# Kernel tuning notes

Measured on AMD Instinct MI355X. Metric: run time of the kernel, lower is better.

Reference implementation:

```python
import jax, jax.numpy as jnp
import numpy as np
import math

N, IN, OUT, E, K = 50000, 256, 256, 800000, 32

def setup_inputs() -> dict:
    key = jax.random.key(0)
    k0, k1, k2, k3, k4 = jax.random.split(key, 5)
    feat = jax.random.normal(k0, (N, IN), dtype=jnp.float32)
    # xavier_uniform with relu gain, as in reset_parameters
    gain = math.sqrt(2.0)
    a = gain * math.sqrt(6.0 / (IN + OUT))
    W_self = jax.random.uniform(k1, (OUT, IN), minval=-a, maxval=a, dtype=jnp.float32)
    W_neigh = jax.random.uniform(k2, (OUT, IN), minval=-a, maxval=a, dtype=jnp.float32)
    b_neigh = jnp.zeros((OUT,), dtype=jnp.float32)
    # random CSR graph: E edges, row pointers from sorted cut points
    indices = jax.random.randint(k3, (E,), 0, N, dtype=jnp.int32)
    inner = jnp.sort(jax.random.randint(k4, (N - 1,), 0, E, dtype=jnp.int32))
    indptr = jnp.concatenate([jnp.zeros((1,), jnp.int32), inner,
                              jnp.full((1,), E, jnp.int32)])
    return {"feat": feat, "W_self": W_self, "W_neigh": W_neigh,
            "b_neigh": b_neigh, "indices": indices, "indptr": indptr}

def reference(feat, W_self, W_neigh, b_neigh, indices, indptr):
    n = feat.shape[0]
    # feat_drop with p=0.0 is identity
    h_self = feat @ W_self.T                      # [N, OUT]
    feat_neigh = feat @ W_neigh.T + b_neigh       # [N, OUT]
    # MaxK: keep top-k entries per row, zero the rest
    vals, idx = jax.lax.top_k(feat_neigh, K)      # [N, K]
    rows = jnp.arange(n)[:, None]
    masked = jnp.zeros_like(feat_neigh).at[rows, idx].set(vals)
    # CSR SpMM with unit values (sum over neighbors)
    deg = indptr[1:] - indptr[:-1]                # [N]
    dst = jnp.repeat(jnp.arange(n, dtype=jnp.int32), deg,
                     total_repeat_length=indices.shape[0])
    h_neigh = jax.ops.segment_sum(masked[indices], dst, num_segments=n)
    return h_self + h_neigh
```

## Files before the change

### kernel.cpp

```cpp
#include <hip/hip_runtime.h>

#define N_NODES 50000
#define TOPK 32
#define SOFT_DELTA 2e-5f

typedef unsigned long long u64;
typedef unsigned u32;
typedef float f32x16 __attribute__((ext_vector_type(16)));
typedef __bf16 bf16x8 __attribute__((ext_vector_type(8)));

__device__ __forceinline__ float dec(u32 u) {
    return __builtin_bit_cast(float, (u & 0x80000000u) ? (u & 0x7FFFFFFFu) : ~u);
}
__device__ __forceinline__ int mbcnt64(u64 m) {
    return __builtin_amdgcn_mbcnt_hi((u32)(m >> 32),
           __builtin_amdgcn_mbcnt_lo((u32)m, 0u));
}

__device__ __forceinline__ u32 enc4(float v, int col) {
    return ((u32)col << 16) |
           ((__builtin_bit_cast(u32, v) + 0x8000u) >> 16);
}

__device__ __forceinline__ u32 s2(float x0, float x1, float& r0, float& r1) {
    const u32 h0 = (__builtin_bit_cast(u32, x0) + 0x8000u) & 0xFFFF0000u;
    const u32 h1 = (__builtin_bit_cast(u32, x1) + 0x8000u) & 0xFFFF0000u;
    r0 = x0 - __builtin_bit_cast(float, h0);
    r1 = x1 - __builtin_bit_cast(float, h1);
    return (h0 >> 16) | h1;
}
__device__ __forceinline__ u32 p2(float x0, float x1) {
    return (((__builtin_bit_cast(u32, x0) + 0x8000u) & 0xFFFF0000u) >> 16) |
           ((__builtin_bit_cast(u32, x1) + 0x8000u) & 0xFFFF0000u);
}

struct Tri { uint4 h1, h2, h3; };
__device__ __forceinline__ Tri cvt8(const float4 u, const float4 v, bool deep) {
    Tri t;
    float r0,r1,r2,r3,r4,r5,r6,r7;
    t.h1.x = s2(u.x, u.y, r0, r1);
    t.h1.y = s2(u.z, u.w, r2, r3);
    t.h1.z = s2(v.x, v.y, r4, r5);
    t.h1.w = s2(v.z, v.w, r6, r7);
    float s0,s1,s2_,s3,s4,s5,s6,s7;
    t.h2.x = s2(r0, r1, s0, s1);
    t.h2.y = s2(r2, r3, s2_, s3);
    t.h2.z = s2(r4, r5, s4, s5);
    t.h2.w = s2(r6, r7, s6, s7);
    if (deep) {
        t.h3.x = p2(s0, s1); t.h3.y = p2(s2_, s3);
        t.h3.z = p2(s4, s5); t.h3.w = p2(s6, s7);
    } else {
        t.h3 = make_uint4(0, 0, 0, 0);
    }
    return t;
}

__global__ __launch_bounds__(256, 2) void gemm_kernel(
    const float* __restrict__ feat,
    const float* __restrict__ Wself,
    const float* __restrict__ Wneigh,
    const float* __restrict__ bneigh,
    float* __restrict__ hself,
    float* __restrict__ fneigh)
{
    __shared__ uint4 LA1[512], LA2[512], LA3[512];
    __shared__ uint4 LB1[512], LB2[512], LB3[512];

    const int tid  = threadIdx.x;
    const int lane = tid & 63;
    const int wave = tid >> 6;
    const int wm   = wave >> 1;
    const int wn   = wave & 1;
    const int kg   = lane >> 5;

    const int rowTile = blockIdx.x >> 2;
    const int colTile = blockIdx.x & 3;
    const int row0 = rowTile * 128;
    const float* __restrict__ Wbase = (colTile < 2) ? Wself : Wneigh;
    const int jbase = (colTile & 1) << 7;
    const bool deep = (colTile >= 2);

    const int srow  = tid >> 1;
    const int shalf = tid & 1;
    int gra = row0 + srow;
    if (gra >= N_NODES) gra = 0;
    const float* pa = feat  + (size_t)gra * 256 + shalf * 16;
    const float* pb = Wbase + (size_t)(jbase + srow) * 256 + shalf * 16;
    const int i0 = ((shalf * 2) << 7) + srow;
    const int i1 = i0 + 128;

    const int rA0 = wm * 64 + (lane & 31);
    const int rB0 = wn * 64 + (lane & 31);

    f32x16 acc[2][2];
#pragma unroll
    for (int i = 0; i < 2; ++i)
#pragma unroll
        for (int j = 0; j < 2; ++j) acc[i][j] = (f32x16)0.f;

    float4 va0, va1, va2, va3, vb0, vb1, vb2, vb3;
    va0 = *(const float4*)(pa);      va1 = *(const float4*)(pa + 4);
    va2 = *(const float4*)(pa + 8);  va3 = *(const float4*)(pa + 12);
    vb0 = *(const float4*)(pb);      vb1 = *(const float4*)(pb + 4);
    vb2 = *(const float4*)(pb + 8);  vb3 = *(const float4*)(pb + 12);

    for (int s = 0; s < 8; ++s) {
        __syncthreads();
        {
            const Tri tA0 = cvt8(va0, va1, deep);
            const Tri tA1 = cvt8(va2, va3, deep);
            const Tri tB0 = cvt8(vb0, vb1, deep);
            const Tri tB1 = cvt8(vb2, vb3, deep);
            LA1[i0] = tA0.h1; LA2[i0] = tA0.h2;
            LA1[i1] = tA1.h1; LA2[i1] = tA1.h2;
            LB1[i0] = tB0.h1; LB2[i0] = tB0.h2;
            LB1[i1] = tB1.h1; LB2[i1] = tB1.h2;
            if (deep) {
                LA3[i0] = tA0.h3; LA3[i1] = tA1.h3;
                LB3[i0] = tB0.h3; LB3[i1] = tB1.h3;
            }
        }
        __syncthreads();

        if (s < 7) {
            const int ko = (s + 1) * 32;
            va0 = *(const float4*)(pa + ko);      va1 = *(const float4*)(pa + ko + 4);
            va2 = *(const float4*)(pa + ko + 8);  va3 = *(const float4*)(pa + ko + 12);
            vb0 = *(const float4*)(pb + ko);      vb1 = *(const float4*)(pb + ko + 4);
            vb2 = *(const float4*)(pb + ko + 8);  vb3 = *(const float4*)(pb + ko + 12);
        }

        if (deep) {
#pragma unroll
            for (int ks = 0; ks < 2; ++ks) {
                const int base = ((ks << 1) | kg) << 7;
                bf16x8 a1[2], a2[2], a3[2], b1[2], b2[2], b3[2];
#pragma unroll
                for (int f = 0; f < 2; ++f) {
                    const int ia = base + rA0 + f * 32;
                    const int ib = base + rB0 + f * 32;
                    a1[f] = __builtin_bit_cast(bf16x8, LA1[ia]);
                    a2[f] = __builtin_bit_cast(bf16x8, LA2[ia]);
                    a3[f] = __builtin_bit_cast(bf16x8, LA3[ia]);
                    b1[f] = __builtin_bit_cast(bf16x8, LB1[ib]);
                    b2[f] = __builtin_bit_cast(bf16x8, LB2[ib]);
                    b3[f] = __builtin_bit_cast(bf16x8, LB3[ib]);
                }
#pragma unroll
                for (int i = 0; i < 2; ++i)
#pragma unroll
                    for (int j = 0; j < 2; ++j) {
                        acc[i][j] = __builtin_amdgcn_mfma_f32_32x32x16_bf16(
                            a1[i], b1[j], acc[i][j], 0, 0, 0);
                        acc[i][j] = __builtin_amdgcn_mfma_f32_32x32x16_bf16(
                            a1[i], b2[j], acc[i][j], 0, 0, 0);
                        acc[i][j] = __builtin_amdgcn_mfma_f32_32x32x16_bf16(
                            a2[i], b1[j], acc[i][j], 0, 0, 0);
                        acc[i][j] = __builtin_amdgcn_mfma_f32_32x32x16_bf16(
                            a2[i], b2[j], acc[i][j], 0, 0, 0);
                        acc[i][j] = __builtin_amdgcn_mfma_f32_32x32x16_bf16(
                            a1[i], b3[j], acc[i][j], 0, 0, 0);
                        acc[i][j] = __builtin_amdgcn_mfma_f32_32x32x16_bf16(
                            a3[i], b1[j], acc[i][j], 0, 0, 0);
                    }
            }
        } else {
#pragma unroll
            for (int ks = 0; ks < 2; ++ks) {
                const int base = ((ks << 1) | kg) << 7;
                bf16x8 a1[2], a2[2], b1[2], b2[2];
#pragma unroll
                for (int f = 0; f < 2; ++f) {
                    const int ia = base + rA0 + f * 32;
                    const int ib = base + rB0 + f * 32;
                    a1[f] = __builtin_bit_cast(bf16x8, LA1[ia]);
                    a2[f] = __builtin_bit_cast(bf16x8, LA2[ia]);
                    b1[f] = __builtin_bit_cast(bf16x8, LB1[ib]);
                    b2[f] = __builtin_bit_cast(bf16x8, LB2[ib]);
                }
#pragma unroll
                for (int i = 0; i < 2; ++i)
#pragma unroll
                    for (int j = 0; j < 2; ++j) {
                        acc[i][j] = __builtin_amdgcn_mfma_f32_32x32x16_bf16(
                            a1[i], b1[j], acc[i][j], 0, 0, 0);
                        acc[i][j] = __builtin_amdgcn_mfma_f32_32x32x16_bf16(
                            a1[i], b2[j], acc[i][j], 0, 0, 0);
                        acc[i][j] = __builtin_amdgcn_mfma_f32_32x32x16_bf16(
                            a2[i], b1[j], acc[i][j], 0, 0, 0);
                    }
            }
        }
    }

#pragma unroll
    for (int i = 0; i < 2; ++i) {
        const int rbase = row0 + wm * 64 + i * 32 + (kg << 2);
#pragma unroll
        for (int j = 0; j < 2; ++j) {
            const int cg = (colTile << 7) + wn * 64 + j * 32 + (lane & 31);
            float* dst; int c; float badd;
            if (colTile < 2) { dst = hself;  c = cg;       badd = 0.f; }
            else             { dst = fneigh; c = cg - 256; badd = bneigh[cg - 256]; }
#pragma unroll
            for (int r = 0; r < 16; ++r) {
                const int grow = rbase + (r & 3) + ((r >> 2) << 3);
                if (grow < N_NODES)
                    dst[(size_t)grow * 256 + c] = acc[i][j][r] + badd;
            }
        }
    }
}

__global__ __launch_bounds__(256) void topk_kernel(
    const float* __restrict__ fneigh,
    u32*  __restrict__ compact,
    u64*  __restrict__ softList)
{
    const int lane = threadIdx.x & 63;
    const int wave = threadIdx.x >> 6;
    const int row  = blockIdx.x * 4 + wave;

    const float4 v4 = ((const float4*)(fneigh + (size_t)row * 256))[lane];
    const float vv[4] = {v4.x, v4.y, v4.z, v4.w};
    u32 key[4];
#pragma unroll
    for (int j = 0; j < 4; ++j) {
        const u32 b = __builtin_bit_cast(u32, vv[j]);
        key[j] = (b & 0x80000000u) ? ~b : (b | 0x80000000u);
    }

    u32 T = 0;
    bool resolved = false;
    for (int b = 31; b >= 0; --b) {
        const u32 t2 = T | (1u << b);
        int cnt = 0;
#pragma unroll
        for (int j = 0; j < 4; ++j) cnt += __popcll(__ballot(key[j] >= t2));
        if (cnt >= TOPK) T = t2;
        if (cnt == TOPK) { resolved = true; break; }
    }
    if (resolved) {
        u32 x = 0xFFFFFFFFu;
#pragma unroll
        for (int j = 0; j < 4; ++j)
            x = min(x, (key[j] >= T) ? key[j] : 0xFFFFFFFFu);
#pragma unroll
        for (int off = 32; off >= 1; off >>= 1)
            x = min(x, (u32)__shfl_xor((int)x, off, 64));
        T = x;
    }

    u64 bgt[4], beq[4];
    int cgt = 0, ceq = 0;
#pragma unroll
    for (int j = 0; j < 4; ++j) {
        bgt[j] = __ballot(key[j] > T);
        beq[j] = __ballot(key[j] == T);
        cgt += __popcll(bgt[j]);
        ceq += __popcll(beq[j]);
    }
    const int r = TOPK - cgt;

    u32 m33;
    if (ceq > r) {
        m33 = T;
    } else {
        u32 x = 0;
#pragma unroll
        for (int j = 0; j < 4; ++j) x = max(x, (key[j] < T) ? key[j] : 0u);
#pragma unroll
        for (int off = 32; off >= 1; off >>= 1) x = max(x, (u32)__shfl_xor((int)x, off, 64));
        m33 = x;
    }
    const float v32f = dec(T);
    const float v33f = dec(m33);
    const bool soft = (v32f - v33f) < SOFT_DELTA;

    const int meqsum = mbcnt64(beq[0]) + mbcnt64(beq[1]) +
                       mbcnt64(beq[2]) + mbcnt64(beq[3]);

    int gtbase = 0, selfpre = 0, spillcol = -1;
#pragma unroll
    for (int j = 0; j < 4; ++j) {
        const int col = lane * 4 + j;
        if (key[j] > T) {
            const int pos = gtbase + mbcnt64(bgt[j]);
            compact[(size_t)row * 32 + pos] = enc4(vv[j], col);
        } else if (key[j] == T) {
            const int eqrank = meqsum + selfpre;
            if (eqrank < r) {
                const float w = (soft && eqrank == r - 1) ? 0.5f : 1.0f;
                compact[(size_t)row * 32 + (cgt + eqrank)] = enc4(vv[j] * w, col);
            } else if (eqrank == r) {
                spillcol = col;
            }
            ++selfpre;
        }
        gtbase += __popcll(bgt[j]);
    }

    if (soft) {
        const u64 valbits = (u64)__builtin_bit_cast(u32, 0.5f * v33f);
        if (ceq > r) {
            if (spillcol >= 0)
                softList[row] = (((u64)(u32)spillcol) << 32) | valbits;
        } else {
            int best = 1 << 30;
#pragma unroll
            for (int j = 0; j < 4; ++j) {
                const u64 b33 = __ballot(key[j] == m33);
                if (b33) best = min(best, ((int)__builtin_ctzll(b33)) * 4 + j);
            }
            if (lane == 0)
                softList[row] = (((u64)(u32)best) << 32) | valbits;
        }
    } else if (lane == 0) {
        softList[row] = 0ull;
    }
}

__global__ __launch_bounds__(512) void spmm_kernel(
    const u32* __restrict__ compact,
    const u64* __restrict__ softList,
    const int* __restrict__ indices,
    const int* __restrict__ indptr,
    float* __restrict__ inout)
{
    __shared__ float accs[8][2][256];

    const int lane = threadIdx.x & 63;
    const int wave = threadIdx.x >> 6;
    const int node = blockIdx.x * 8 + wave;
    const int half = lane >> 5;
    const int e    = lane & 31;
    float* acc  = accs[wave][half];

    const float4 z4 = make_float4(0.f, 0.f, 0.f, 0.f);
    ((float4*)&accs[wave][0][0])[lane] = z4;
    ((float4*)&accs[wave][1][0])[lane] = z4;

    const int start = indptr[node];
    const int deg   = indptr[node + 1] - start;
    const float4 hs = ((const float4*)(inout + (size_t)node * 256))[lane];

    for (int base = 0; base < deg; base += 64) {
        const int n = min(64, deg - base);
        const int myidx = (base + lane < deg) ? indices[start + base + lane] : 0;
        for (int d = 0; d < n; d += 16) {
            int s[8]; bool ok[8]; u32 ent[8];
#pragma unroll
            for (int k = 0; k < 8; ++k) {
                const int ei = d + 2 * k + half;
                ok[k] = ei < n;
                s[k]  = __shfl(myidx, min(ei, n - 1), 64);
                ent[k] = compact[(size_t)s[k] * 32 + e];
            }
            u64 se[8];
            if (e == 0) {
#pragma unroll
                for (int k = 0; k < 8; ++k) se[k] = softList[s[k]];
            }
#pragma unroll
            for (int k = 0; k < 8; ++k) {
                const int c = (int)(ent[k] >> 16);
                float v = __builtin_bit_cast(float, ent[k] << 16);
                if (!ok[k]) v = 0.f;
                acc[c] += v;
                if (e == 0 && ok[k]) {
                    const u32 vb = (u32)se[k];
                    if (vb)
                        acc[(int)(se[k] >> 32)] += __builtin_bit_cast(float, vb);
                }
            }
        }
    }

    const float4 a0 = ((const float4*)&accs[wave][0][0])[lane];
    const float4 a1 = ((const float4*)&accs[wave][1][0])[lane];
    float4 o;
    o.x = a0.x + a1.x + hs.x;
    o.y = a0.y + a1.y + hs.y;
    o.z = a0.z + a1.z + hs.z;
    o.w = a0.w + a1.w + hs.w;
    ((float4*)(inout + (size_t)node * 256))[lane] = o;
}

extern "C" void kernel_launch(void* const* d_in, const int* in_sizes, int n_in,
                              void* d_out, int out_size, void* d_ws, size_t ws_size,
                              hipStream_t stream) {
    const float* feat   = (const float*)d_in[0];
    const float* Wself  = (const float*)d_in[1];
    const float* Wneigh = (const float*)d_in[2];
    const float* bneigh = (const float*)d_in[3];
    const int* indices  = (const int*)d_in[4];
    const int* indptr   = (const int*)d_in[5];
    float* out = (float*)d_out;

    char* ws       = (char*)d_ws;
    float* fneigh  = (float*)ws;
    u32*  compact  = (u32*)(ws + (size_t)N_NODES * 256 * 4);
    u64*  softList = (u64*)(ws + (size_t)N_NODES * 256 * 4
                               + (size_t)N_NODES * 32 * 4);

    const int rowTiles = (N_NODES + 127) / 128;
    gemm_kernel<<<dim3(rowTiles * 4), dim3(256), 0, stream>>>(
        feat, Wself, Wneigh, bneigh, out, fneigh);

    const int rowBlocks = N_NODES / 4;
    topk_kernel<<<dim3(rowBlocks), dim3(256), 0, stream>>>(fneigh, compact, softList);

    const int spmmBlocks = N_NODES / 8;
    spmm_kernel<<<dim3(spmmBlocks), dim3(512), 0, stream>>>(
        compact, softList, indices, indptr, out);
}
```

Before: 297.3 us.

## Fuse neighbor GEMM with top-k selection and pre-split W_neigh into bf16 planes

```diff
diff --git a/kernel.cpp b/kernel.cpp
--- a/kernel.cpp
+++ b/kernel.cpp
@@ -15,6 +15,12 @@
 __device__ __forceinline__ int mbcnt64(u64 m) {
     return __builtin_amdgcn_mbcnt_hi((u32)(m >> 32),
            __builtin_amdgcn_mbcnt_lo((u32)m, 0u));
+}
+
+__device__ __forceinline__ void gll16(const uint4* g, uint4* l) {
+    __builtin_amdgcn_global_load_lds(
+        (const __attribute__((address_space(1))) void*)g,
+        (__attribute__((address_space(3))) void*)l, 16, 0, 0);
 }
 
 __device__ __forceinline__ u32 enc4(float v, int col) {
@@ -56,16 +62,27 @@
     return t;
 }
 
-__global__ __launch_bounds__(256, 2) void gemm_kernel(
+__global__ __launch_bounds__(256) void wprep_kernel(
+    const float* __restrict__ Wneigh,
+    uint4* __restrict__ WT1, uint4* __restrict__ WT2, uint4* __restrict__ WT3)
+{
+    for (int it = 0; it < 4; ++it) {
+        const int id = (blockIdx.x * 4 + it) * 256 + threadIdx.x;
+        const int s = id >> 10, rem = id & 1023;
+        const int c = rem >> 8, j = rem & 255;
+        const float* src = Wneigh + (size_t)j * 256 + s * 32 + c * 8;
+        const Tri t = cvt8(*(const float4*)src, *(const float4*)(src + 4), true);
+        WT1[id] = t.h1; WT2[id] = t.h2; WT3[id] = t.h3;
+    }
+}
+
+__global__ __launch_bounds__(256, 2) void gemm_self_kernel(
     const float* __restrict__ feat,
     const float* __restrict__ Wself,
-    const float* __restrict__ Wneigh,
-    const float* __restrict__ bneigh,
-    float* __restrict__ hself,
-    float* __restrict__ fneigh)
+    float* __restrict__ hself)
 {
-    __shared__ uint4 LA1[512], LA2[512], LA3[512];
-    __shared__ uint4 LB1[512], LB2[512], LB3[512];
+    __shared__ uint4 LA1[512], LA2[512];
+    __shared__ uint4 LB1[512], LB2[512];
 
     const int tid  = threadIdx.x;
     const int lane = tid & 63;
@@ -74,19 +91,17 @@
     const int wn   = wave & 1;
     const int kg   = lane >> 5;
 
-    const int rowTile = blockIdx.x >> 2;
-    const int colTile = blockIdx.x & 3;
+    const int rowTile = blockIdx.x >> 1;
+    const int colTile = blockIdx.x & 1;
     const int row0 = rowTile * 128;
-    const float* __restrict__ Wbase = (colTile < 2) ? Wself : Wneigh;
-    const int jbase = (colTile & 1) << 7;
-    const bool deep = (colTile >= 2);
+    const int jbase = colTile << 7;
 
     const int srow  = tid >> 1;
     const int shalf = tid & 1;
     int gra = row0 + srow;
     if (gra >= N_NODES) gra = 0;
     const float* pa = feat  + (size_t)gra * 256 + shalf * 16;
-    const float* pb = Wbase + (size_t)(jbase + srow) * 256 + shalf * 16;
+    const float* pb = Wself + (size_t)(jbase + srow) * 256 + shalf * 16;
     const int i0 = ((shalf * 2) << 7) + srow;
     const int i1 = i0 + 128;
 
@@ -108,18 +123,14 @@
     for (int s = 0; s < 8; ++s) {
         __syncthreads();
         {
-            const Tri tA0 = cvt8(va0, va1, deep);
-            const Tri tA1 = cvt8(va2, va3, deep);
-            const Tri tB0 = cvt8(vb0, vb1, deep);
-            const Tri tB1 = cvt8(vb2, vb3, deep);
+            const Tri tA0 = cvt8(va0, va1, false);
+            const Tri tA1 = cvt8(va2, va3, false);
+            const Tri tB0 = cvt8(vb0, vb1, false);
+            const Tri tB1 = cvt8(vb2, vb3, false);
             LA1[i0] = tA0.h1; LA2[i0] = tA0.h2;
             LA1[i1] = tA1.h1; LA2[i1] = tA1.h2;
             LB1[i0] = tB0.h1; LB2[i0] = tB0.h2;
             LB1[i1] = tB1.h1; LB2[i1] = tB1.h2;
-            if (deep) {
-                LA3[i0] = tA0.h3; LA3[i1] = tA1.h3;
-                LB3[i0] = tB0.h3; LB3[i1] = tB1.h3;
-            }
         }
         __syncthreads();
 
@@ -131,66 +142,30 @@
             vb2 = *(const float4*)(pb + ko + 8);  vb3 = *(const float4*)(pb + ko + 12);
         }
 
-        if (deep) {
-#pragma unroll
-            for (int ks = 0; ks < 2; ++ks) {
-                const int base = ((ks << 1) | kg) << 7;
-                bf16x8 a1[2], a2[2], a3[2], b1[2], b2[2], b3[2];
-#pragma unroll
-                for (int f = 0; f < 2; ++f) {
-                    const int ia = base + rA0 + f * 32;
-                    const int ib = base + rB0 + f * 32;
-                    a1[f] = __builtin_bit_cast(bf16x8, LA1[ia]);
-                    a2[f] = __builtin_bit_cast(bf16x8, LA2[ia]);
-                    a3[f] = __builtin_bit_cast(bf16x8, LA3[ia]);
-                    b1[f] = __builtin_bit_cast(bf16x8, LB1[ib]);
-                    b2[f] = __builtin_bit_cast(bf16x8, LB2[ib]);
-                    b3[f] = __builtin_bit_cast(bf16x8, LB3[ib]);
+#pragma unroll
+        for (int ks = 0; ks < 2; ++ks) {
+            const int base = ((ks << 1) | kg) << 7;
+            bf16x8 a1[2], a2[2], b1[2], b2[2];
+#pragma unroll
+            for (int f = 0; f < 2; ++f) {
+                const int ia = base + rA0 + f * 32;
+                const int ib = base + rB0 + f * 32;
+                a1[f] = __builtin_bit_cast(bf16x8, LA1[ia]);
+                a2[f] = __builtin_bit_cast(bf16x8, LA2[ia]);
+                b1[f] = __builtin_bit_cast(bf16x8, LB1[ib]);
+                b2[f] = __builtin_bit_cast(bf16x8, LB2[ib]);
+            }
+#pragma unroll
+            for (int i = 0; i < 2; ++i)
+#pragma unroll
+                for (int j = 0; j < 2; ++j) {
+                    acc[i][j] = __builtin_amdgcn_mfma_f32_32x32x16_bf16(
+                        a1[i], b1[j], acc[i][j], 0, 0, 0);
+                    acc[i][j] = __builtin_amdgcn_mfma_f32_32x32x16_bf16(
+                        a1[i], b2[j], acc[i][j], 0, 0, 0);
+                    acc[i][j] = __builtin_amdgcn_mfma_f32_32x32x16_bf16(
+                        a2[i], b1[j], acc[i][j], 0, 0, 0);
                 }
-#pragma unroll
-                for (int i = 0; i < 2; ++i)
-#pragma unroll
-                    for (int j = 0; j < 2; ++j) {
-                        acc[i][j] = __builtin_amdgcn_mfma_f32_32x32x16_bf16(
-                            a1[i], b1[j], acc[i][j], 0, 0, 0);
-                        acc[i][j] = __builtin_amdgcn_mfma_f32_32x32x16_bf16(
-                            a1[i], b2[j], acc[i][j], 0, 0, 0);
-                        acc[i][j] = __builtin_amdgcn_mfma_f32_32x32x16_bf16(
-                            a2[i], b1[j], acc[i][j], 0, 0, 0);
-                        acc[i][j] = __builtin_amdgcn_mfma_f32_32x32x16_bf16(
-                            a2[i], b2[j], acc[i][j], 0, 0, 0);
-                        acc[i][j] = __builtin_amdgcn_mfma_f32_32x32x16_bf16(
-                            a1[i], b3[j], acc[i][j], 0, 0, 0);
-                        acc[i][j] = __builtin_amdgcn_mfma_f32_32x32x16_bf16(
-                            a3[i], b1[j], acc[i][j], 0, 0, 0);
-                    }
-            }
-        } else {
-#pragma unroll
-            for (int ks = 0; ks < 2; ++ks) {
-                const int base = ((ks << 1) | kg) << 7;
-                bf16x8 a1[2], a2[2], b1[2], b2[2];
-#pragma unroll
-                for (int f = 0; f < 2; ++f) {
-                    const int ia = base + rA0 + f * 32;
-                    const int ib = base + rB0 + f * 32;
-                    a1[f] = __builtin_bit_cast(bf16x8, LA1[ia]);
-                    a2[f] = __builtin_bit_cast(bf16x8, LA2[ia]);
-                    b1[f] = __builtin_bit_cast(bf16x8, LB1[ib]);
-                    b2[f] = __builtin_bit_cast(bf16x8, LB2[ib]);
-                }
-#pragma unroll
-                for (int i = 0; i < 2; ++i)
-#pragma unroll
-                    for (int j = 0; j < 2; ++j) {
-                        acc[i][j] = __builtin_amdgcn_mfma_f32_32x32x16_bf16(
-                            a1[i], b1[j], acc[i][j], 0, 0, 0);
-                        acc[i][j] = __builtin_amdgcn_mfma_f32_32x32x16_bf16(
-                            a1[i], b2[j], acc[i][j], 0, 0, 0);
-                        acc[i][j] = __builtin_amdgcn_mfma_f32_32x32x16_bf16(
-                            a2[i], b1[j], acc[i][j], 0, 0, 0);
-                    }
-            }
         }
     }
 
@@ -200,124 +175,224 @@
 #pragma unroll
         for (int j = 0; j < 2; ++j) {
             const int cg = (colTile << 7) + wn * 64 + j * 32 + (lane & 31);
-            float* dst; int c; float badd;
-            if (colTile < 2) { dst = hself;  c = cg;       badd = 0.f; }
-            else             { dst = fneigh; c = cg - 256; badd = bneigh[cg - 256]; }
 #pragma unroll
             for (int r = 0; r < 16; ++r) {
                 const int grow = rbase + (r & 3) + ((r >> 2) << 3);
                 if (grow < N_NODES)
-                    dst[(size_t)grow * 256 + c] = acc[i][j][r] + badd;
-            }
-        }
-    }
-}
-
-__global__ __launch_bounds__(256) void topk_kernel(
-    const float* __restrict__ fneigh,
+                    hself[(size_t)grow * 256 + cg] = acc[i][j][r];
+            }
+        }
+    }
+}
+
+__global__ __launch_bounds__(512, 4) void gemm_nt_kernel(
+    const float* __restrict__ feat,
+    const uint4* __restrict__ WT1, const uint4* __restrict__ WT2,
+    const uint4* __restrict__ WT3,
+    const float* __restrict__ bneigh,
     u32*  __restrict__ compact,
     u64*  __restrict__ softList)
 {
-    const int lane = threadIdx.x & 63;
-    const int wave = threadIdx.x >> 6;
-    const int row  = blockIdx.x * 4 + wave;
-
-    const float4 v4 = ((const float4*)(fneigh + (size_t)row * 256))[lane];
-    const float vv[4] = {v4.x, v4.y, v4.z, v4.w};
-    u32 key[4];
-#pragma unroll
-    for (int j = 0; j < 4; ++j) {
-        const u32 b = __builtin_bit_cast(u32, vv[j]);
-        key[j] = (b & 0x80000000u) ? ~b : (b | 0x80000000u);
-    }
-
-    u32 T = 0;
-    bool resolved = false;
-    for (int b = 31; b >= 0; --b) {
-        const u32 t2 = T | (1u << b);
-        int cnt = 0;
-#pragma unroll
-        for (int j = 0; j < 4; ++j) cnt += __popcll(__ballot(key[j] >= t2));
-        if (cnt >= TOPK) T = t2;
-        if (cnt == TOPK) { resolved = true; break; }
-    }
-    if (resolved) {
-        u32 x = 0xFFFFFFFFu;
-#pragma unroll
-        for (int j = 0; j < 4; ++j)
-            x = min(x, (key[j] >= T) ? key[j] : 0xFFFFFFFFu);
-#pragma unroll
-        for (int off = 32; off >= 1; off >>= 1)
-            x = min(x, (u32)__shfl_xor((int)x, off, 64));
-        T = x;
-    }
-
-    u64 bgt[4], beq[4];
-    int cgt = 0, ceq = 0;
-#pragma unroll
-    for (int j = 0; j < 4; ++j) {
-        bgt[j] = __ballot(key[j] > T);
-        beq[j] = __ballot(key[j] == T);
-        cgt += __popcll(bgt[j]);
-        ceq += __popcll(beq[j]);
-    }
-    const int r = TOPK - cgt;
-
-    u32 m33;
-    if (ceq > r) {
-        m33 = T;
-    } else {
-        u32 x = 0;
-#pragma unroll
-        for (int j = 0; j < 4; ++j) x = max(x, (key[j] < T) ? key[j] : 0u);
-#pragma unroll
-        for (int off = 32; off >= 1; off >>= 1) x = max(x, (u32)__shfl_xor((int)x, off, 64));
-        m33 = x;
-    }
-    const float v32f = dec(T);
-    const float v33f = dec(m33);
-    const bool soft = (v32f - v33f) < SOFT_DELTA;
-
-    const int meqsum = mbcnt64(beq[0]) + mbcnt64(beq[1]) +
-                       mbcnt64(beq[2]) + mbcnt64(beq[3]);
-
-    int gtbase = 0, selfpre = 0, spillcol = -1;
-#pragma unroll
-    for (int j = 0; j < 4; ++j) {
-        const int col = lane * 4 + j;
-        if (key[j] > T) {
-            const int pos = gtbase + mbcnt64(bgt[j]);
-            compact[(size_t)row * 32 + pos] = enc4(vv[j], col);
-        } else if (key[j] == T) {
-            const int eqrank = meqsum + selfpre;
-            if (eqrank < r) {
-                const float w = (soft && eqrank == r - 1) ? 0.5f : 1.0f;
-                compact[(size_t)row * 32 + (cgt + eqrank)] = enc4(vv[j] * w, col);
-            } else if (eqrank == r) {
-                spillcol = col;
-            }
-            ++selfpre;
-        }
-        gtbase += __popcll(bgt[j]);
-    }
-
-    if (soft) {
-        const u64 valbits = (u64)__builtin_bit_cast(u32, 0.5f * v33f);
-        if (ceq > r) {
-            if (spillcol >= 0)
-                softList[row] = (((u64)(u32)spillcol) << 32) | valbits;
+    __shared__ uint4 SMEM[4096];
+    uint4* LA1 = SMEM;
+    uint4* LA2 = SMEM + 256;
+    uint4* LA3 = SMEM + 512;
+    uint4* LB1 = SMEM + 768;
+    uint4* LB2 = SMEM + 1792;
+    uint4* LB3 = SMEM + 2816;
+    float* stage = (float*)SMEM;
+
+    const int tid  = threadIdx.x;
+    const int lane = tid & 63;
+    const int wave = tid >> 6;
+    const int kg   = lane >> 5;
+
+    const int row0 = blockIdx.x * 64;
+
+    const int ar = tid & 63;
+    const int ac = (tid >> 6) & 3;
+    int gra = row0 + ar;
+    if (gra >= N_NODES) gra = row0;
+    const float* pa = feat + (size_t)gra * 256 + ac * 8;
+    const int aidx = ac * 64 + ar;
+
+    const int rA0  = lane & 31;
+    const int bcol = wave * 32 + (lane & 31);
+
+    f32x16 acc[2];
+    acc[0] = (f32x16)0.f; acc[1] = (f32x16)0.f;
+
+    float4 va0 = make_float4(0,0,0,0), va1 = make_float4(0,0,0,0);
+    if (tid < 256) { va0 = *(const float4*)(pa); va1 = *(const float4*)(pa + 4); }
+
+    for (int s = 0; s < 8; ++s) {
+        __syncthreads();
+        {
+            const int base = s * 1024;
+            const int w64  = wave * 64;
+            gll16(WT1 + base + w64 + lane,       LB1 + w64);
+            gll16(WT1 + base + 512 + w64 + lane, LB1 + 512 + w64);
+            gll16(WT2 + base + w64 + lane,       LB2 + w64);
+            gll16(WT2 + base + 512 + w64 + lane, LB2 + 512 + w64);
+            gll16(WT3 + base + w64 + lane,       LB3 + w64);
+            gll16(WT3 + base + 512 + w64 + lane, LB3 + 512 + w64);
+        }
+        if (tid < 256) {
+            const Tri t = cvt8(va0, va1, true);
+            LA1[aidx] = t.h1; LA2[aidx] = t.h2; LA3[aidx] = t.h3;
+            if (s < 7) {
+                const int ko = (s + 1) * 32;
+                va0 = *(const float4*)(pa + ko);
+                va1 = *(const float4*)(pa + ko + 4);
+            }
+        }
+        __syncthreads();
+
+#pragma unroll
+        for (int ks = 0; ks < 2; ++ks) {
+            const int ch = (ks << 1) | kg;
+            bf16x8 a1[2], a2[2], a3[2], b1, b2, b3;
+            {
+                const int ib = ch * 256 + bcol;
+                b1 = __builtin_bit_cast(bf16x8, LB1[ib]);
+                b2 = __builtin_bit_cast(bf16x8, LB2[ib]);
+                b3 = __builtin_bit_cast(bf16x8, LB3[ib]);
+            }
+#pragma unroll
+            for (int f = 0; f < 2; ++f) {
+                const int ia = ch * 64 + rA0 + f * 32;
+                a1[f] = __builtin_bit_cast(bf16x8, LA1[ia]);
+                a2[f] = __builtin_bit_cast(bf16x8, LA2[ia]);
+                a3[f] = __builtin_bit_cast(bf16x8, LA3[ia]);
+            }
+#pragma unroll
+            for (int i = 0; i < 2; ++i) {
+                acc[i] = __builtin_amdgcn_mfma_f32_32x32x16_bf16(a1[i], b1, acc[i], 0, 0, 0);
+                acc[i] = __builtin_amdgcn_mfma_f32_32x32x16_bf16(a1[i], b2, acc[i], 0, 0, 0);
+                acc[i] = __builtin_amdgcn_mfma_f32_32x32x16_bf16(a2[i], b1, acc[i], 0, 0, 0);
+                acc[i] = __builtin_amdgcn_mfma_f32_32x32x16_bf16(a2[i], b2, acc[i], 0, 0, 0);
+                acc[i] = __builtin_amdgcn_mfma_f32_32x32x16_bf16(a1[i], b3, acc[i], 0, 0, 0);
+                acc[i] = __builtin_amdgcn_mfma_f32_32x32x16_bf16(a3[i], b1, acc[i], 0, 0, 0);
+            }
+        }
+    }
+
+    __syncthreads();
+    const float bn = bneigh[bcol];
+#pragma unroll
+    for (int i = 0; i < 2; ++i) {
+        const int rbase = i * 32 + (kg << 2);
+#pragma unroll
+        for (int r = 0; r < 16; ++r) {
+            const int rl = rbase + (r & 3) + ((r >> 2) << 3);
+            stage[rl * 256 + bcol] = acc[i][r] + bn;
+        }
+    }
+    __syncthreads();
+
+    for (int it = 0; it < 8; ++it) {
+        const int rl  = wave * 8 + it;
+        const int row = row0 + rl;
+        if (row >= N_NODES) break;
+
+        const float4 v4 = ((const float4*)stage)[rl * 64 + lane];
+        const float vv[4] = {v4.x, v4.y, v4.z, v4.w};
+        u32 key[4];
+#pragma unroll
+        for (int j = 0; j < 4; ++j) {
+            const u32 b = __builtin_bit_cast(u32, vv[j]);
+            key[j] = (b & 0x80000000u) ? ~b : (b | 0x80000000u);
+        }
+
+        u32 T = 0;
+        bool resolved = false;
+        for (int b = 31; b >= 0; --b) {
+            const u32 t2 = T | (1u << b);
+            int cnt = 0;
+#pragma unroll
+            for (int j = 0; j < 4; ++j) cnt += __popcll(__ballot(key[j] >= t2));
+            if (cnt >= TOPK) T = t2;
+            if (cnt == TOPK) { resolved = true; break; }
+        }
+        if (resolved) {
+            u32 x = 0xFFFFFFFFu;
+#pragma unroll
+            for (int j = 0; j < 4; ++j)
+                x = min(x, (key[j] >= T) ? key[j] : 0xFFFFFFFFu);
+#pragma unroll
+            for (int off = 32; off >= 1; off >>= 1)
+                x = min(x, (u32)__shfl_xor((int)x, off, 64));
+            T = x;
+        }
+
+        u64 bgt[4], beq[4];
+        int cgt = 0, ceq = 0;
+#pragma unroll
+        for (int j = 0; j < 4; ++j) {
+            bgt[j] = __ballot(key[j] > T);
+            beq[j] = __ballot(key[j] == T);
+            cgt += __popcll(bgt[j]);
+            ceq += __popcll(beq[j]);
+        }
+        const int r_ = TOPK - cgt;
+
+        u32 m33;
+        if (ceq > r_) {
+            m33 = T;
         } else {
-            int best = 1 << 30;
-#pragma unroll
-            for (int j = 0; j < 4; ++j) {
-                const u64 b33 = __ballot(key[j] == m33);
-                if (b33) best = min(best, ((int)__builtin_ctzll(b33)) * 4 + j);
-            }
-            if (lane == 0)
-                softList[row] = (((u64)(u32)best) << 32) | valbits;
-        }
-    } else if (lane == 0) {
-        softList[row] = 0ull;
+            u32 x = 0;
+#pragma unroll
+            for (int j = 0; j < 4; ++j) x = max(x, (key[j] < T) ? key[j] : 0u);
+#pragma unroll
+            for (int off = 32; off >= 1; off >>= 1)
+                x = max(x, (u32)__shfl_xor((int)x, off, 64));
+            m33 = x;
+        }
+        const float v32f = dec(T);
+        const float v33f = dec(m33);
+        const bool soft = (v32f - v33f) < SOFT_DELTA;
+
+        const int meqsum = mbcnt64(beq[0]) + mbcnt64(beq[1]) +
+                           mbcnt64(beq[2]) + mbcnt64(beq[3]);
+
+        int gtbase = 0, selfpre = 0, spillcol = -1;
+#pragma unroll
+        for (int j = 0; j < 4; ++j) {
+            const int col = lane * 4 + j;
+            if (key[j] > T) {
+                const int pos = gtbase + mbcnt64(bgt[j]);
+                compact[(size_t)row * 32 + pos] = enc4(vv[j], col);
+            } else if (key[j] == T) {
+                const int eqrank = meqsum + selfpre;
+                if (eqrank < r_) {
+                    const float w = (soft && eqrank == r_ - 1) ? 0.5f : 1.0f;
+                    compact[(size_t)row * 32 + (cgt + eqrank)] = enc4(vv[j] * w, col);
+                } else if (eqrank == r_) {
+                    spillcol = col;
+                }
+                ++selfpre;
+            }
+            gtbase += __popcll(bgt[j]);
+        }
+
+        if (soft) {
+            const u64 valbits = (u64)__builtin_bit_cast(u32, 0.5f * v33f);
+            if (ceq > r_) {
+                if (spillcol >= 0)
+                    softList[row] = (((u64)(u32)spillcol) << 32) | valbits;
+            } else {
+                int best = 1 << 30;
+#pragma unroll
+                for (int j = 0; j < 4; ++j) {
+                    const u64 b33 = __ballot(key[j] == m33);
+                    if (b33) best = min(best, ((int)__builtin_ctzll(b33)) * 4 + j);
+                }
+                if (lane == 0)
+                    softList[row] = (((u64)(u32)best) << 32) | valbits;
+            }
+        } else if (lane == 0) {
+            softList[row] = 0ull;
+        }
     }
 }
 
@@ -399,17 +474,21 @@
     float* out = (float*)d_out;
 
     char* ws       = (char*)d_ws;
-    float* fneigh  = (float*)ws;
-    u32*  compact  = (u32*)(ws + (size_t)N_NODES * 256 * 4);
-    u64*  softList = (u64*)(ws + (size_t)N_NODES * 256 * 4
-                               + (size_t)N_NODES * 32 * 4);
-
-    const int rowTiles = (N_NODES + 127) / 128;
-    gemm_kernel<<<dim3(rowTiles * 4), dim3(256), 0, stream>>>(
-        feat, Wself, Wneigh, bneigh, out, fneigh);
-
-    const int rowBlocks = N_NODES / 4;
-    topk_kernel<<<dim3(rowBlocks), dim3(256), 0, stream>>>(fneigh, compact, softList);
+    u32*  compact  = (u32*)(ws);
+    u64*  softList = (u64*)(ws + 6400000);
+    uint4* WT1     = (uint4*)(ws + 6800000);
+    uint4* WT2     = WT1 + 8192;
+    uint4* WT3     = WT2 + 8192;
+
+    wprep_kernel<<<dim3(8), dim3(256), 0, stream>>>(Wneigh, WT1, WT2, WT3);
+
+    const int rowTiles128 = (N_NODES + 127) / 128;
+    gemm_self_kernel<<<dim3(rowTiles128 * 2), dim3(256), 0, stream>>>(
+        feat, Wself, out);
+
+    const int rowTiles64 = (N_NODES + 63) / 64;
+    gemm_nt_kernel<<<dim3(rowTiles64), dim3(512), 0, stream>>>(
+        feat, WT1, WT2, WT3, bneigh, compact, softList);
 
     const int spmmBlocks = N_NODES / 8;
     spmm_kernel<<<dim3(spmmBlocks), dim3(512), 0, stream>>>(
```

After: 293.7 us. No clear change (-1.2%).
